# Kernel optimization log

Hardware: AMD Instinct MI355X
Metric: run time of the kernel (lower is better)

The kernel has to match this reference:

```python
import jax, jax.numpy as jnp
import numpy as np

B, N, V, X, H, C = 128, 1023, 32000, 256, 256, 10  # N = 2^10 - 1 perfect binary tree (heap layout)


def setup_inputs() -> dict:
    key = jax.random.key(0)
    ks = jax.random.split(key, 12)
    s = 0.02
    return {
        "wordid": jax.random.randint(ks[0], (B, N), 0, V),
        "h0": jnp.zeros((B, N, H), jnp.float32),
        "c0": jnp.zeros((B, N, H), jnp.float32),
        "emb": jax.random.normal(ks[1], (V, X), jnp.float32) * s,
        "W_iou": jax.random.normal(ks[2], (3 * H, X), jnp.float32) * s,
        "U_iou": jax.random.normal(ks[3], (3 * H, 2 * H), jnp.float32) * s,
        "b_iou": jnp.zeros((1, 3 * H), jnp.float32),
        "Uf_W": jax.random.normal(ks[4], (2 * H, 2 * H), jnp.float32) * s,
        "Uf_b": jnp.zeros((2 * H,), jnp.float32),
        "Wmem": jax.random.normal(ks[5], (H, H), jnp.float32) * s,
        "wh_W": jax.random.normal(ks[6], (H, H), jnp.float32) * s,
        "wh_b": jnp.zeros((H,), jnp.float32),
        "lin_W": jax.random.normal(ks[7], (C, H), jnp.float32) * s,
        "lin_b": jnp.zeros((C,), jnp.float32),
    }


def _apply_node(iou, b_iou, c_in):
    # TreeLSTMCell.apply_node_func: iou -> i,o,u gates; c = sig(i)*tanh(u) + c_in; h = sig(o)*tanh(c)
    i, o, u = jnp.split(iou + b_iou, 3, axis=-1)
    c = jax.nn.sigmoid(i) * jnp.tanh(u) + c_in
    h = jax.nn.sigmoid(o) * jnp.tanh(c)
    return h, c


def reference(wordid, h0, c0, emb, W_iou, U_iou, b_iou, Uf_W, Uf_b, Wmem, wh_W, wh_b, lin_W, lin_b):
    Bn, Nn, Hn = h0.shape
    D = int(np.log2(Nn + 1))  # depth of perfect binary tree
    h, c = h0, c0
    # --- leaves (frontier 0): iou = W_iou(embed), c from initial state ---
    s = 2 ** (D - 1) - 1
    x_leaf = emb[wordid[:, s:]]                                  # [B, Nleaf, X]
    iou = jnp.einsum('bnx,gx->bng', x_leaf, W_iou)               # [B, Nleaf, 3H]
    hl, cl = _apply_node(iou, b_iou, c[:, s:])
    h = h.at[:, s:].set(hl)
    c = c.at[:, s:].set(cl)
    # --- internal levels, bottom-up (reduce_func overwrites iou and c) ---
    for level in range(D - 2, -1, -1):
        ps, pe = 2 ** level - 1, 2 ** (level + 1) - 1
        npar = pe - ps
        cs, ce = pe, pe + 2 * npar  # children of parent p live at 2p+1, 2p+2 (contiguous block)
        h_cat = h[:, cs:ce].reshape(Bn, npar, 2 * Hn)            # [B, npar, 2H]
        f = jax.nn.sigmoid(jnp.einsum('bnk,jk->bnj', h_cat, Uf_W) + Uf_b)
        f = f.reshape(Bn, npar, 2, Hn)
        c_sum = jnp.sum(f * c[:, cs:ce].reshape(Bn, npar, 2, Hn), axis=2)
        iou_p = jnp.einsum('bnk,gk->bng', h_cat, U_iou)          # [B, npar, 3H]
        hp, cp = _apply_node(iou_p, b_iou, c_sum)
        h = h.at[:, ps:pe].set(hp)
        c = c.at[:, ps:pe].set(cp)
    # --- TreeAttention: root (node 0 per tree) attends over all nodes of its tree ---
    dec = h[:, 0]                                                # [B, H]
    proj = jnp.einsum('bnh,gh->bng', h, Wmem)                    # memory_project
    scores = jnp.einsum('bh,bnh->bn', dec, proj)
    attn = jax.nn.softmax(scores, axis=1)                        # MaskedSoftmax, mask=None
    context = jnp.einsum('bn,bnh->bh', attn, h)                  # [B, H]
    hid = jax.nn.relu(context @ wh_W.T + wh_b)
    return hid @ lin_W.T + lin_b                                 # [B, num_classes]
```

## Files before the change

kernel.cpp:

```cpp
#include <hip/hip_runtime.h>
#include <math.h>

#define BB      128
#define NNODES  1023
#define HD      256
#define LEAVES  512
#define IOU3    768
#define CAT2    512
#define LDCOMB  1280

typedef unsigned short ushort_t;
typedef __bf16 bf16x8 __attribute__((ext_vector_type(8)));
typedef float  f32x4  __attribute__((ext_vector_type(4)));

__device__ __forceinline__ float sigf(float x) { return 1.0f / (1.0f + expf(-x)); }

__device__ __forceinline__ void split_bf16(float x, ushort_t& h, ushort_t& l)
{
    unsigned u = __float_as_uint(x);
    unsigned r = u + 0x7fff + ((u >> 16) & 1);
    h = (ushort_t)(r >> 16);
    float fh = __uint_as_float((unsigned)h << 16);
    float d = x - fh;
    unsigned u2 = __float_as_uint(d);
    unsigned r2 = u2 + 0x7fff + ((u2 >> 16) & 1);
    l = (ushort_t)(r2 >> 16);
}

__device__ __forceinline__ float rh2(ushort_t h, ushort_t l)
{
    return __uint_as_float((unsigned)h << 16) + __uint_as_float((unsigned)l << 16);
}

__global__ void k_split4(const float* __restrict__ src, ushort_t* __restrict__ hi,
                         ushort_t* __restrict__ lo, int n4)
{
    int i = blockIdx.x * 256 + threadIdx.x;
    if (i >= n4) return;
    float4 v = ((const float4*)src)[i];
    ushort4 hv, lv;
    split_bf16(v.x, hv.x, lv.x);
    split_bf16(v.y, hv.y, lv.y);
    split_bf16(v.z, hv.z, lv.z);
    split_bf16(v.w, hv.w, lv.w);
    ((ushort4*)hi)[i] = hv;
    ((ushort4*)lo)[i] = lv;
}

__global__ void k_build_wcat(const float* __restrict__ Uf, const float* __restrict__ Ui,
                             ushort_t* __restrict__ hi, ushort_t* __restrict__ lo)
{
    int i = blockIdx.x * 256 + threadIdx.x;
    if (i >= 1280 * 128) return;
    int row = i >> 7, c4 = i & 127;
    const float* src = (row < 512) ? (Uf + (size_t)row * 512)
                                   : (Ui + (size_t)(row - 512) * 512);
    float4 v = ((const float4*)src)[c4];
    ushort4 hv, lv;
    split_bf16(v.x, hv.x, lv.x);
    split_bf16(v.y, hv.y, lv.y);
    split_bf16(v.z, hv.z, lv.z);
    split_bf16(v.w, hv.w, lv.w);
    ((ushort4*)hi)[i] = hv;
    ((ushort4*)lo)[i] = lv;
}

#define BM 128
#define BN 128
#define BK 32

__global__ __launch_bounds__(512, 4)
void gemm_mfma(const ushort_t* __restrict__ Ahi, const ushort_t* __restrict__ Alo,
               const int* __restrict__ ids,
               int lognpar, unsigned sB, int sP, int m0, int K,
               const ushort_t* __restrict__ Bhi, const ushort_t* __restrict__ Blo,
               float* __restrict__ C, int ldc)
{
    __shared__ __align__(16) char lds[65536];
    const int tid = threadIdx.x;

    int bx = blockIdx.x, by = blockIdx.y;
    {
        const int gx = gridDim.x, gy = gridDim.y;
        if ((gx & 7) == 0) {
            int f = by * gx + bx;
            int span = gy << 3;
            int s = f / span;
            int wv = f - s * span;
            bx = (s << 3) + (wv & 7);
            by = wv >> 3;
        }
    }

    const int srow = tid >> 2, sko = tid & 3;
    unsigned aoff, boff;
    {
        int mg = m0 + bx * BM + srow;
        unsigned ab;
        if (ids) {
            ab = (unsigned)ids[mg] * (unsigned)K;
        } else {
            int b = mg >> lognpar;
            int p = mg & ((1 << lognpar) - 1);
            ab = (unsigned)b * sB + (unsigned)p * (unsigned)sP;
        }
        aoff = ab + sko * 8;
        boff = (unsigned)(by * BN + srow) * (unsigned)K + sko * 8;
    }
    const int wofs = srow * 64 + ((sko ^ ((srow >> 1) & 3)) << 4);

    uint4 rAh, rAl, rBh, rBl;
    auto LOADT = [&](int k0) {
        rAh = *(const uint4*)(Ahi + aoff + k0);
        rAl = *(const uint4*)(Alo + aoff + k0);
        rBh = *(const uint4*)(Bhi + boff + k0);
        rBl = *(const uint4*)(Blo + boff + k0);
    };
    auto STORE = [&](int buf) {
        char* b = lds + buf * 32768;
        *(uint4*)(b +     0 + wofs) = rAh;
        *(uint4*)(b +  8192 + wofs) = rAl;
        *(uint4*)(b + 16384 + wofs) = rBh;
        *(uint4*)(b + 24576 + wofs) = rBl;
    };

    const int w = tid >> 6, lane = tid & 63;
    const int wm = w >> 2, wn = w & 3;
    const int rA0 = wm * 64 + (lane & 15);
    const int rB0 = wn * 32 + (lane & 15);
    const int ko = lane >> 4;
    const int rdA = rA0 * 64 + ((ko ^ ((rA0 >> 1) & 3)) << 4);
    const int rdB = rB0 * 64 + ((ko ^ ((rB0 >> 1) & 3)) << 4);

    f32x4 acc[4][2];
#pragma unroll
    for (int mi = 0; mi < 4; ++mi)
#pragma unroll
        for (int ni = 0; ni < 2; ++ni) acc[mi][ni] = (f32x4){0.f, 0.f, 0.f, 0.f};

    const int nt = K / BK;
    LOADT(0);
    STORE(0);
    __syncthreads();
    int cur = 0;
    for (int t = 0; t < nt; ++t) {
        if (t + 1 < nt) LOADT((t + 1) * BK);
        char* base = lds + cur * 32768;
        bf16x8 ah[4], al[4], bh[2], bl[2];
#pragma unroll
        for (int f = 0; f < 4; ++f) {
            ah[f] = *(const bf16x8*)(base +        rdA + f * 1024);
            al[f] = *(const bf16x8*)(base + 8192 + rdA + f * 1024);
        }
#pragma unroll
        for (int f = 0; f < 2; ++f) {
            bh[f] = *(const bf16x8*)(base + 16384 + rdB + f * 1024);
            bl[f] = *(const bf16x8*)(base + 24576 + rdB + f * 1024);
        }
        __builtin_amdgcn_s_setprio(1);
#pragma unroll
        for (int mi = 0; mi < 4; ++mi)
#pragma unroll
            for (int ni = 0; ni < 2; ++ni) {
                acc[mi][ni] = __builtin_amdgcn_mfma_f32_16x16x32_bf16(ah[mi], bh[ni], acc[mi][ni], 0, 0, 0);
                acc[mi][ni] = __builtin_amdgcn_mfma_f32_16x16x32_bf16(ah[mi], bl[ni], acc[mi][ni], 0, 0, 0);
                acc[mi][ni] = __builtin_amdgcn_mfma_f32_16x16x32_bf16(al[mi], bh[ni], acc[mi][ni], 0, 0, 0);
            }
        __builtin_amdgcn_s_setprio(0);
        if (t + 1 < nt) STORE(cur ^ 1);
        __syncthreads();
        cur ^= 1;
    }

    {
        char* patch = lds + w * 2304;
        const int cl = lane & 15, rg = lane >> 4;
        const int gcol0 = by * BN + wn * 32;
#pragma unroll
        for (int mi = 0; mi < 4; ++mi) {
#pragma unroll
            for (int ni = 0; ni < 2; ++ni)
#pragma unroll
                for (int r = 0; r < 4; ++r)
                    *(float*)(patch + (rg * 4 + r) * 144 + (ni * 16 + cl) * 4) = acc[mi][ni][r];
            int grow0 = bx * BM + wm * 64 + mi * 16;
#pragma unroll
            for (int i = 0; i < 2; ++i) {
                int slot = lane + 64 * i;
                int lr = slot >> 3, c4 = slot & 7;
                f32x4 vv = *(const f32x4*)(patch + lr * 144 + c4 * 16);
                *(f32x4*)(C + (size_t)(grow0 + lr) * ldc + gcol0 + c4 * 4) = vv;
            }
        }
    }
}

__global__ void k_leaf_ids(const int* __restrict__ wordid, int* __restrict__ ids)
{
    int idx = blockIdx.x * 256 + threadIdx.x;
    int b = idx >> 9, leaf = idx & 511;
    ids[idx] = wordid[b * NNODES + 511 + leaf];
}

__global__ void k_apply_leaf(const float* __restrict__ buf, const float* __restrict__ b_iou,
                             const float* __restrict__ c0,
                             ushort_t* __restrict__ hhi, ushort_t* __restrict__ hlo,
                             float* __restrict__ c, int m0)
{
    int idx = blockIdx.x * 256 + threadIdx.x;
    int m_l = idx >> 8, hh = idx & 255;
    int mg = m0 + m_l;
    int b = mg >> 9, leaf = mg & 511;
    int node = 511 + leaf;
    const float* br = buf + (size_t)m_l * IOU3;
    float iv = br[hh]        + b_iou[hh];
    float ov = br[256 + hh]  + b_iou[256 + hh];
    float uv = br[512 + hh]  + b_iou[512 + hh];
    size_t nb = ((size_t)b * NNODES + node) * HD + hh;
    float cn = sigf(iv) * tanhf(uv) + c0[nb];
    float hn = sigf(ov) * tanhf(cn);
    c[nb] = cn;
    split_bf16(hn, hhi[nb], hlo[nb]);
}

__global__ void k_apply_level(const float* __restrict__ buf, const float* __restrict__ b_iou,
                              const float* __restrict__ Uf_b,
                              ushort_t* __restrict__ hhi, ushort_t* __restrict__ hlo,
                              float* __restrict__ c,
                              int m0, int lognpar, int ps, int cs)
{
    int idx = blockIdx.x * 256 + threadIdx.x;
    int m_l = idx >> 8, hh = idx & 255;
    int mg = m0 + m_l;
    int b = mg >> lognpar;
    int p = mg & ((1 << lognpar) - 1);
    const float* br = buf + (size_t)m_l * LDCOMB;
    float fl = sigf(br[hh]        + Uf_b[hh]);
    float fr = sigf(br[256 + hh]  + Uf_b[256 + hh]);
    size_t cb = ((size_t)b * NNODES + cs + 2 * p) * HD + hh;
    float csum = fl * c[cb] + fr * c[cb + HD];
    float iv = br[512 + hh]  + b_iou[hh];
    float ov = br[768 + hh]  + b_iou[256 + hh];
    float uv = br[1024 + hh] + b_iou[512 + hh];
    float cn = sigf(iv) * tanhf(uv) + csum;
    float hn = sigf(ov) * tanhf(cn);
    size_t pb = ((size_t)b * NNODES + ps + p) * HD + hh;
    c[pb] = cn;
    split_bf16(hn, hhi[pb], hlo[pb]);
}

__global__ void k_dec_v(const ushort_t* __restrict__ hhi, const ushort_t* __restrict__ hlo,
                        const float* __restrict__ Wmem, float* __restrict__ v)
{
    int b = blockIdx.x, k = threadIdx.x;
    __shared__ float dec[HD];
    size_t base = (size_t)b * NNODES * HD;
    dec[k] = rh2(hhi[base + k], hlo[base + k]);
    __syncthreads();
    float s = 0.f;
    for (int g = 0; g < HD; ++g) s = fmaf(dec[g], Wmem[g * HD + k], s);
    v[b * HD + k] = s;
}

__global__ void k_scores(const ushort_t* __restrict__ hhi, const ushort_t* __restrict__ hlo,
                         const float* __restrict__ v, float* __restrict__ scores)
{
    int b = blockIdx.x;
    int w = threadIdx.x >> 6, lane = threadIdx.x & 63;
    int n = blockIdx.y * 4 + w;
    if (n >= NNODES) return;
    size_t hb = ((size_t)b * NNODES + n) * HD;
    ushort4 ph = *(const ushort4*)(hhi + hb + lane * 4);
    ushort4 pl = *(const ushort4*)(hlo + hb + lane * 4);
    float4 vv = *(const float4*)(v + b * HD + lane * 4);
    float s = rh2(ph.x, pl.x) * vv.x + rh2(ph.y, pl.y) * vv.y +
              rh2(ph.z, pl.z) * vv.z + rh2(ph.w, pl.w) * vv.w;
#pragma unroll
    for (int o = 32; o; o >>= 1) s += __shfl_down(s, o);
    if (lane == 0) scores[(size_t)b * NNODES + n] = s;
}

__global__ void k_softmax(const float* __restrict__ scores, float* __restrict__ attn)
{
    int b = blockIdx.x, t = threadIdx.x;
    __shared__ float red[4];
    float sv[4];
    float m = -INFINITY;
#pragma unroll
    for (int i = 0; i < 4; ++i) {
        int n = t + 256 * i;
        sv[i] = (n < NNODES) ? scores[(size_t)b * NNODES + n] : -INFINITY;
        m = fmaxf(m, sv[i]);
    }
#pragma unroll
    for (int o = 32; o; o >>= 1) m = fmaxf(m, __shfl_xor(m, o));
    int w = t >> 6, lane = t & 63;
    if (lane == 0) red[w] = m;
    __syncthreads();
    m = fmaxf(fmaxf(red[0], red[1]), fmaxf(red[2], red[3]));
    float s = 0.f;
#pragma unroll
    for (int i = 0; i < 4; ++i) {
        int n = t + 256 * i;
        sv[i] = (n < NNODES) ? expf(sv[i] - m) : 0.f;
        s += sv[i];
    }
#pragma unroll
    for (int o = 32; o; o >>= 1) s += __shfl_xor(s, o);
    __syncthreads();
    if (lane == 0) red[w] = s;
    __syncthreads();
    s = red[0] + red[1] + red[2] + red[3];
    float inv = 1.0f / s;
#pragma unroll
    for (int i = 0; i < 4; ++i) {
        int n = t + 256 * i;
        if (n < NNODES) attn[(size_t)b * NNODES + n] = sv[i] * inv;
    }
}

__global__ void k_context(const ushort_t* __restrict__ hhi, const ushort_t* __restrict__ hlo,
                          const float* __restrict__ attn, float* __restrict__ partial)
{
    int b = blockIdx.x, ch = blockIdx.y, k = threadIdx.x;
    int n0 = ch * 128;
    int n1 = n0 + 128; if (n1 > NNODES) n1 = NNODES;
    float s = 0.f;
    for (int n = n0; n < n1; ++n) {
        size_t i = ((size_t)b * NNODES + n) * HD + k;
        s = fmaf(attn[(size_t)b * NNODES + n], rh2(hhi[i], hlo[i]), s);
    }
    partial[((size_t)b * 8 + ch) * HD + k] = s;
}

__global__ void k_final(const float* __restrict__ partial,
                        const float* __restrict__ wh_W, const float* __restrict__ wh_b,
                        const float* __restrict__ lin_W, const float* __restrict__ lin_b,
                        float* __restrict__ out)
{
    int b = blockIdx.x, j = threadIdx.x;
    __shared__ float ctx[HD];
    __shared__ float hid[HD];
    float s = 0.f;
#pragma unroll
    for (int ch = 0; ch < 8; ++ch) s += partial[((size_t)b * 8 + ch) * HD + j];
    ctx[j] = s;
    __syncthreads();
    float a = wh_b[j];
    for (int k = 0; k < HD; ++k) a = fmaf(ctx[k], wh_W[j * HD + k], a);
    hid[j] = fmaxf(a, 0.f);
    __syncthreads();
    if (j < 10) {
        float o = lin_b[j];
        for (int k = 0; k < HD; ++k) o = fmaf(hid[k], lin_W[j * HD + k], o);
        out[b * 10 + j] = o;
    }
}

extern "C" void kernel_launch(void* const* d_in, const int* in_sizes, int n_in,
                              void* d_out, int out_size, void* d_ws, size_t ws_size,
                              hipStream_t stream)
{
    const int*   wordid = (const int*)d_in[0];
    const float* c0     = (const float*)d_in[2];
    const float* emb    = (const float*)d_in[3];
    const float* W_iou  = (const float*)d_in[4];
    const float* U_iou  = (const float*)d_in[5];
    const float* b_iou  = (const float*)d_in[6];
    const float* Uf_W   = (const float*)d_in[7];
    const float* Uf_b   = (const float*)d_in[8];
    const float* Wmem   = (const float*)d_in[9];
    const float* wh_W   = (const float*)d_in[10];
    const float* wh_b   = (const float*)d_in[11];
    const float* lin_W  = (const float*)d_in[12];
    const float* lin_b  = (const float*)d_in[13];
    float* out = (float*)d_out;

    const int V = in_sizes[3] / 256;
    const size_t nh = (size_t)BB * NNODES * HD;

    char* ws = (char*)d_ws;
    size_t off = 0;
    auto alloc = [&](size_t bytes) -> void* {
        void* p = ws + off;
        off += (bytes + 255) & ~(size_t)255;
        return p;
    };
    ushort_t* hhi  = (ushort_t*)alloc(nh * 2);
    ushort_t* hlo  = (ushort_t*)alloc(nh * 2);
    float*    c    = (float*)   alloc(nh * 4);
    ushort_t* ehi  = (ushort_t*)alloc((size_t)V * 256 * 2);
    ushort_t* elo  = (ushort_t*)alloc((size_t)V * 256 * 2);
    ushort_t* wchi = (ushort_t*)alloc((size_t)LDCOMB * 512 * 2);
    ushort_t* wclo = (ushort_t*)alloc((size_t)LDCOMB * 512 * 2);
    ushort_t* wihi = (ushort_t*)alloc((size_t)IOU3 * 256 * 2);
    ushort_t* wilo = (ushort_t*)alloc((size_t)IOU3 * 256 * 2);
    int*   ids     = (int*)  alloc((size_t)BB * LEAVES * 4);
    float* v       = (float*)alloc((size_t)BB * HD * 4);
    float* scores  = (float*)alloc((size_t)BB * NNODES * 4);
    float* attn    = (float*)alloc((size_t)BB * NNODES * 4);
    float* partial = (float*)alloc((size_t)BB * 8 * HD * 4);

    size_t remain = (ws_size > off) ? (ws_size - off) : 0;
    size_t rows = remain / (LDCOMB * 4);
    int CH = (int)((rows > 16384) ? 16384 : rows);
    CH &= ~127;
    if (CH < 128) CH = 128;
    float* buf = (float*)alloc((size_t)CH * LDCOMB * 4);

    k_split4<<<(V * 256 / 4 + 255) / 256, 256, 0, stream>>>(emb, ehi, elo, V * 256 / 4);
    k_build_wcat<<<(1280 * 128 + 255) / 256, 256, 0, stream>>>(Uf_W, U_iou, wchi, wclo);
    k_split4<<<(IOU3 * 256 / 4 + 255) / 256, 256, 0, stream>>>(W_iou, wihi, wilo, IOU3 * 256 / 4);
    k_leaf_ids<<<(BB * LEAVES) / 256, 256, 0, stream>>>(wordid, ids);

    {
        int M = BB * LEAVES;
        for (int m0 = 0; m0 < M; m0 += CH) {
            int Mc = M - m0; if (Mc > CH) Mc = CH;
            dim3 g(Mc / BM, IOU3 / BN);
            gemm_mfma<<<g, 512, 0, stream>>>(ehi, elo, ids, 0, 0u, 0, m0, 256,
                                             wihi, wilo, buf, IOU3);
            k_apply_leaf<<<Mc, 256, 0, stream>>>(buf, b_iou, c0, hhi, hlo, c, m0);
        }
    }

    for (int L = 8; L >= 0; --L) {
        int npar = 1 << L;
        int ps = (1 << L) - 1;
        int cs = (1 << (L + 1)) - 1;
        int M = BB * npar;
        unsigned sB = NNODES * HD;
        int sP = 2 * HD;
        const ushort_t* Abh = hhi + (size_t)cs * HD;
        const ushort_t* Abl = hlo + (size_t)cs * HD;
        for (int m0 = 0; m0 < M; m0 += CH) {
            int Mc = M - m0; if (Mc > CH) Mc = CH;
            dim3 g(Mc / BM, LDCOMB / BN);
            gemm_mfma<<<g, 512, 0, stream>>>(Abh, Abl, (const int*)nullptr, L, sB, sP,
                                             m0, CAT2, wchi, wclo, buf, LDCOMB);
            k_apply_level<<<Mc, 256, 0, stream>>>(buf, b_iou, Uf_b, hhi, hlo, c,
                                                  m0, L, ps, cs);
        }
    }

    k_dec_v<<<BB, HD, 0, stream>>>(hhi, hlo, Wmem, v);
    k_scores<<<dim3(BB, 256), 256, 0, stream>>>(hhi, hlo, v, scores);
    k_softmax<<<BB, 256, 0, stream>>>(scores, attn);
    k_context<<<dim3(BB, 8), HD, 0, stream>>>(hhi, hlo, attn, partial);
    k_final<<<BB, HD, 0, stream>>>(partial, wh_W, wh_b, lin_W, lin_b, out);
}
```

Baseline: 780.8 us.

## Stage GEMM tiles via direct global-to-LDS loads with vmcnt-based pipelining

Replaces the register-staged global→LDS tile copy in the split-bf16 MFMA GEMM with global_load_lds direct loads into the next double buffer. Sync moves from __syncthreads to explicit vmcnt waits plus s_barrier. The XOR swizzle now goes on the global source address instead of the LDS write offset, because the direct-to-LDS write is linear per wave. The leaf chunk size cap is also doubled, so fewer GEMM and apply launches run if workspace allows. Risks include hazards from the manual waitcnt, which does not cover the LDS reads of the other buffer, and the larger buffer footprint.

Measured after the change: 741.0 us. -5.1%, faster.

```diff
diff --git a/kernel.cpp b/kernel.cpp
--- a/kernel.cpp
+++ b/kernel.cpp
@@ -14,6 +14,13 @@
 typedef float  f32x4  __attribute__((ext_vector_type(4)));
 
 __device__ __forceinline__ float sigf(float x) { return 1.0f / (1.0f + expf(-x)); }
+
+__device__ __forceinline__ void gload16(const void* g, void* l)
+{
+    __builtin_amdgcn_global_load_lds(
+        (const __attribute__((address_space(1))) unsigned int*)g,
+        (__attribute__((address_space(3))) unsigned int*)l, 16, 0, 0);
+}
 
 __device__ __forceinline__ void split_bf16(float x, ushort_t& h, ushort_t& l)
 {
@@ -92,39 +99,33 @@
         }
     }
 
-    const int srow = tid >> 2, sko = tid & 3;
+    const int w = tid >> 6, lane = tid & 63;
+
     unsigned aoff, boff;
     {
-        int mg = m0 + bx * BM + srow;
+        int row = tid >> 2;
+        int slotp = (tid & 3) ^ ((row >> 1) & 3);
+        int mg = m0 + bx * BM + row;
         unsigned ab;
         if (ids) {
             ab = (unsigned)ids[mg] * (unsigned)K;
         } else {
             int b = mg >> lognpar;
-            int p = mg & ((1 << lognpar) - 1);
-            ab = (unsigned)b * sB + (unsigned)p * (unsigned)sP;
-        }
-        aoff = ab + sko * 8;
-        boff = (unsigned)(by * BN + srow) * (unsigned)K + sko * 8;
-    }
-    const int wofs = srow * 64 + ((sko ^ ((srow >> 1) & 3)) << 4);
-
-    uint4 rAh, rAl, rBh, rBl;
-    auto LOADT = [&](int k0) {
-        rAh = *(const uint4*)(Ahi + aoff + k0);
-        rAl = *(const uint4*)(Alo + aoff + k0);
-        rBh = *(const uint4*)(Bhi + boff + k0);
-        rBl = *(const uint4*)(Blo + boff + k0);
+            int q = mg & ((1 << lognpar) - 1);
+            ab = (unsigned)b * sB + (unsigned)q * (unsigned)sP;
+        }
+        aoff = ab + slotp * 8;
+        boff = (unsigned)(by * BN + row) * (unsigned)K + slotp * 8;
+    }
+    const int wdst = w * 1024;
+
+    auto STAGE = [&](int k0, char* buf) {
+        gload16(Ahi + aoff + k0, buf +     0 + wdst);
+        gload16(Alo + aoff + k0, buf +  8192 + wdst);
+        gload16(Bhi + boff + k0, buf + 16384 + wdst);
+        gload16(Blo + boff + k0, buf + 24576 + wdst);
     };
-    auto STORE = [&](int buf) {
-        char* b = lds + buf * 32768;
-        *(uint4*)(b +     0 + wofs) = rAh;
-        *(uint4*)(b +  8192 + wofs) = rAl;
-        *(uint4*)(b + 16384 + wofs) = rBh;
-        *(uint4*)(b + 24576 + wofs) = rBl;
-    };
-
-    const int w = tid >> 6, lane = tid & 63;
+
     const int wm = w >> 2, wn = w & 3;
     const int rA0 = wm * 64 + (lane & 15);
     const int rB0 = wn * 32 + (lane & 15);
@@ -139,12 +140,17 @@
         for (int ni = 0; ni < 2; ++ni) acc[mi][ni] = (f32x4){0.f, 0.f, 0.f, 0.f};
 
     const int nt = K / BK;
-    LOADT(0);
-    STORE(0);
-    __syncthreads();
+    STAGE(0, lds);
     int cur = 0;
     for (int t = 0; t < nt; ++t) {
-        if (t + 1 < nt) LOADT((t + 1) * BK);
+        if (t + 1 < nt) {
+            STAGE((t + 1) * BK, lds + (cur ^ 1) * 32768);
+            asm volatile("s_waitcnt vmcnt(4)" ::: "memory");
+        } else {
+            asm volatile("s_waitcnt vmcnt(0)" ::: "memory");
+        }
+        __builtin_amdgcn_s_barrier();
+        __builtin_amdgcn_sched_barrier(0);
         char* base = lds + cur * 32768;
         bf16x8 ah[4], al[4], bh[2], bl[2];
 #pragma unroll
@@ -167,8 +173,7 @@
                 acc[mi][ni] = __builtin_amdgcn_mfma_f32_16x16x32_bf16(al[mi], bh[ni], acc[mi][ni], 0, 0, 0);
             }
         __builtin_amdgcn_s_setprio(0);
-        if (t + 1 < nt) STORE(cur ^ 1);
-        __syncthreads();
+        __builtin_amdgcn_s_barrier();
         cur ^= 1;
     }
 
@@ -403,7 +408,7 @@
 
     size_t remain = (ws_size > off) ? (ws_size - off) : 0;
     size_t rows = remain / (LDCOMB * 4);
-    int CH = (int)((rows > 16384) ? 16384 : rows);
+    int CH = (int)((rows > 32768) ? 32768 : rows);
     CH &= ~127;
     if (CH < 128) CH = 128;
     float* buf = (float*)alloc((size_t)CH * LDCOMB * 4);
```
